# Optimization experiments

Hardware: AMD Instinct MI355X
Metric: run time of the kernel (lower is better)

The kernel has to match this reference:

```python
import jax, jax.numpy as jnp
import numpy as np

B, L, H, T, S, D = 64, 512, 768, 256, 128, 8
N = B * S            # 8192 graph nodes total
E = 16 * N           # random edges (avg degree 16)
NPD = N // D         # nodes per document
NEG_SLOPE = 0.2


def setup_inputs() -> dict:
    rng = np.random.default_rng(0)
    key = jax.random.key(0)
    ks = jax.random.split(key, 11)
    features = jax.random.normal(ks[0], (B, L, H), jnp.float32)
    starts = rng.integers(0, L - 8, (B, T))
    lens = rng.integers(1, 9, (B, T))
    token_spans = jnp.asarray(np.stack([starts, starts + lens], -1), jnp.int32)
    masks = jnp.ones((B, L), jnp.int32)
    selected_indices = jnp.asarray(rng.integers(0, T, (B, S)), jnp.int32)
    # edges within each document's node block, plus self loops (dgl.add_self_loop)
    dst0 = rng.integers(0, N, E)
    src0 = (dst0 // NPD) * NPD + rng.integers(0, NPD, E)
    loop = np.arange(N)
    src = jnp.asarray(np.concatenate([src0, loop]), jnp.int32)
    dst = jnp.asarray(np.concatenate([dst0, loop]), jnp.int32)
    spd = B // D
    doc_spans = jnp.asarray(
        np.stack([np.arange(D) * spd, (np.arange(D) + 1) * spd], -1), jnp.int32)
    segment_ids = jnp.asarray(rng.integers(0, 2, (B, L)), jnp.int32)
    is_head = jnp.asarray(rng.integers(0, 3, (B, L)), jnp.int32)
    p = lambda k, shp: jax.random.normal(k, shp, jnp.float32) * 0.05
    out = dict(features=features, token_spans=token_spans, masks=masks,
               selected_indices=selected_indices, src=src, dst=dst,
               doc_spans=doc_spans, segment_ids=segment_ids, is_head=is_head)
    for i in range(3):
        out[f"W{i}"] = p(ks[1 + 3 * i], (H, H))
        out[f"al{i}"] = p(ks[2 + 3 * i], (H,))
        out[f"ar{i}"] = p(ks[3 + 3 * i], (H,))
    return out


def _gat_layer(h, W, al, ar, src, dst, n):
    # DGL GATConv, 1 head: z = Wh; e_ij = LeakyReLU(a_l.z_i + a_r.z_j);
    # edge-softmax over incoming edges of each dst; aggregate; ELU.
    z = h @ W                                   # [N, H]
    el = z @ al                                 # [N]
    er = z @ ar                                 # [N]
    e = jax.nn.leaky_relu(el[src] + er[dst], NEG_SLOPE)
    e = e - jax.ops.segment_max(e, dst, num_segments=n)[dst]
    ex = jnp.exp(e)
    a = ex / jax.ops.segment_sum(ex, dst, num_segments=n)[dst]
    out = jax.ops.segment_sum(a[:, None] * z[src], dst, num_segments=n)
    return jax.nn.elu(out)


def reference(features, W0, al0, ar0, W1, al1, ar1, W2, al2, ar2,
              token_spans, masks, selected_indices, src, dst,
              doc_spans, segment_ids, is_head):
    dt = features.dtype
    # --- AverageSpanExtractor over token spans ---
    pos = jnp.arange(L)
    s = token_spans[..., 0:1]                   # [B,T,1]
    e = token_spans[..., 1:2]
    span_mask = ((pos >= s) & (pos < e) & (masks[:, None, :] > 0)).astype(dt)
    counts = jnp.maximum(span_mask.sum(-1), 1.0)
    token_repr = jnp.einsum('btl,blh->bth', span_mask, features) / counts[..., None]
    token_repr = token_repr * (token_spans[..., 1] > 0).astype(dt)[..., None]
    # --- select graph nodes ---
    sel = jnp.take_along_axis(token_repr, selected_indices[:, :, None], axis=1)
    h = sel.reshape(N, H)
    # --- 3-layer single-head GAT ---
    for (W, al, ar) in ((W0, al0, ar0), (W1, al1, ar1), (W2, al2, ar2)):
        h = _gat_layer(h, W, al, ar, src, dst, N)
    # --- dgl.mean_nodes per document ---
    sent_doc = jnp.searchsorted(doc_spans[:, 0], jnp.arange(B), side='right') - 1
    node_doc = sent_doc[jnp.arange(N) // S]
    node_cnt = jnp.maximum(
        jax.ops.segment_sum(jnp.ones(N, dt), node_doc, num_segments=D), 1.0)
    avg = jax.ops.segment_sum(h, node_doc, num_segments=D) / node_cnt[:, None]
    # --- query features ---
    qmask = ((is_head != 2) & (segment_ids == 0) & (masks > 0)).astype(dt)
    all_q = (features * qmask[..., None]).sum(1)   # [B,H]
    doc_cnt = jnp.maximum((doc_spans[:, 1] - doc_spans[:, 0]).astype(dt), 1.0)
    qf = jax.ops.segment_sum(all_q, sent_doc, num_segments=D) / doc_cnt[:, None]
    # --- L1 pairwise distance per document ---
    return jnp.abs(qf - avg).sum(-1)               # [D]
```

## Files before the change

### kernel.cpp

```cpp
#include <hip/hip_runtime.h>
#include <hip/hip_bf16.h>

constexpr int B_ = 64, L_ = 512, H_ = 768, T_ = 256, S_ = 128, D_ = 8;
constexpr int N_ = B_ * S_;
constexpr int E0_ = 16 * N_;
constexpr int NE_ = E0_ + N_;
constexpr float NEG_SLOPE = 0.2f;
constexpr int KDIM = 768;

typedef __attribute__((ext_vector_type(8))) short short8v;
typedef __attribute__((ext_vector_type(4))) float f32x4;

#define GLOAD_LDS16(g, l) __builtin_amdgcn_global_load_lds( \
    (const __attribute__((address_space(1))) void*)(g), \
    (__attribute__((address_space(3))) void*)(l), 16, 0, 0)

__device__ __forceinline__ float bf2f(short s) {
  unsigned u = ((unsigned)(unsigned short)s) << 16;
  return __builtin_bit_cast(float, u);
}
__device__ __forceinline__ short f2bf(float f) {
  return (short)__bfloat16_as_ushort(__float2bfloat16(f));
}
__device__ __forceinline__ int docof(int b, const int* __restrict__ doc_spans) {
  int cnt = 0;
  for (int dd = 0; dd < D_; dd++) cnt += (doc_spans[dd * 2] <= b) ? 1 : 0;
  return cnt - 1;
}

__global__ __launch_bounds__(256) void k_token_wt(const float* __restrict__ features,
                                                  const int* __restrict__ token_spans,
                                                  const int* __restrict__ masks,
                                                  const int* __restrict__ selidx,
                                                  __hip_bfloat16* __restrict__ h0,
                                                  const float* __restrict__ W0,
                                                  const float* __restrict__ W1,
                                                  const float* __restrict__ W2,
                                                  __hip_bfloat16* __restrict__ Wt) {
  int bid = blockIdx.x;
  if (bid < N_) {
    if (threadIdx.x >= 192) return;
    int n = bid;
    int b = n / S_;
    int t = selidx[n];
    int st = token_spans[(b * T_ + t) * 2 + 0];
    int en = token_spans[(b * T_ + t) * 2 + 1];
    int tid = threadIdx.x;
    float4 a = make_float4(0.f, 0.f, 0.f, 0.f);
    int cnt = 0;
    for (int l = st; l < en; l++) {
      if (masks[b * L_ + l] > 0) {
        cnt++;
        float4 v = ((const float4*)(features + ((size_t)b * L_ + l) * H_))[tid];
        a.x += v.x; a.y += v.y; a.z += v.z; a.w += v.w;
      }
    }
    float sc = (en > 0) ? (1.0f / (float)max(cnt, 1)) : 0.0f;
    short4 o;
    o.x = f2bf(a.x * sc); o.y = f2bf(a.y * sc); o.z = f2bf(a.z * sc); o.w = f2bf(a.w * sc);
    ((short4*)(h0 + (size_t)n * H_))[tid] = o;
    return;
  }
  int wb = bid - N_;
  int layer = wb / 576;
  int rem = wb % 576;
  int k0 = (rem % 24) * 32, n0 = (rem / 24) * 32;
  const float* Ws[3] = {W0, W1, W2};
  const float* W = Ws[layer];
  __hip_bfloat16* O = Wt + (size_t)layer * H_ * H_;
  __shared__ float tbuf[32][33];
  int x = threadIdx.x % 32, y = threadIdx.x / 32;
  for (int i = 0; i < 32; i += 8)
    tbuf[y + i][x] = W[(size_t)(k0 + y + i) * H_ + n0 + x];
  __syncthreads();
  for (int i = 0; i < 32; i += 8)
    O[(size_t)(n0 + y + i) * H_ + k0 + x] = __float2bfloat16(tbuf[x][y + i]);
}

__global__ void k_count(const int* __restrict__ dst, int* __restrict__ counts, int ne) {
  int i = blockIdx.x * 256 + threadIdx.x;
  if (i < ne) atomicAdd(&counts[dst[i]], 1);
}

__global__ __launch_bounds__(1024) void k_scan(const int* __restrict__ counts,
                                               int* __restrict__ offs,
                                               int* __restrict__ cursor) {
  __shared__ int part[1024];
  int tid = threadIdx.x;
  int base = tid * 8;
  int loc[8];
  int s = 0;
  for (int i = 0; i < 8; i++) { loc[i] = s; s += counts[base + i]; }
  part[tid] = s;
  __syncthreads();
  for (int off = 1; off < 1024; off <<= 1) {
    int v = (tid >= off) ? part[tid - off] : 0;
    __syncthreads();
    part[tid] += v;
    __syncthreads();
  }
  int excl = (tid == 0) ? 0 : part[tid - 1];
  for (int i = 0; i < 8; i++) {
    int o = excl + loc[i];
    offs[base + i] = o;
    cursor[base + i] = o;
  }
  if (tid == 1023) offs[N_] = part[1023];
}

__global__ void k_scatter(const int* __restrict__ dst, const int* __restrict__ src,
                          int* __restrict__ cursor, int* __restrict__ esrc, int ne) {
  int i = blockIdx.x * 256 + threadIdx.x;
  if (i < ne) { int p = atomicAdd(&cursor[dst[i]], 1); esrc[p] = src[i]; }
}

__global__ __launch_bounds__(256) void k_gemm_bf16(const __hip_bfloat16* __restrict__ A,
                                                   const __hip_bfloat16* __restrict__ Bt,
                                                   __hip_bfloat16* __restrict__ C,
                                                   const float* __restrict__ al,
                                                   const float* __restrict__ ar,
                                                   float* __restrict__ el,
                                                   float* __restrict__ er) {
  __shared__ __hip_bfloat16 As[2][128 * 32];
  __shared__ __hip_bfloat16 Bs[2][128 * 32];
  int tid = threadIdx.x;
  int bm = blockIdx.x * 128;
  int bn = blockIdx.y * 128;
  int w = tid >> 6;
  int l = tid & 63;
  int wr = w >> 1, wc = w & 1;
  int lr = l & 15;
  int lk = (l >> 4) * 8;
  f32x4 acc[4][4] = {};

  const __hip_bfloat16* gA[2];
  const __hip_bfloat16* gB[2];
  int ldsoff[2];
#pragma unroll
  for (int i = 0; i < 2; i++) {
    int idx = i * 256 + tid;
    int row = idx >> 2;
    int ck = (idx & 3) * 8;
    gA[i] = A + (size_t)(bm + row) * KDIM + ck;
    gB[i] = Bt + (size_t)(bn + row) * KDIM + ck;
    ldsoff[i] = idx * 8;
  }

  auto stage = [&](int buf, int k0) {
#pragma unroll
    for (int i = 0; i < 2; i++) GLOAD_LDS16(gA[i] + k0, &As[buf][ldsoff[i]]);
#pragma unroll
    for (int i = 0; i < 2; i++) GLOAD_LDS16(gB[i] + k0, &Bs[buf][ldsoff[i]]);
  };

  stage(0, 0);
  __syncthreads();

  constexpr int NT = KDIM / 32;
  for (int t = 0; t < NT; t++) {
    int cur = t & 1;
    if (t < NT - 1) stage(cur ^ 1, (t + 1) * 32);
    short8v a_frag[4], b_frag[4];
#pragma unroll
    for (int m = 0; m < 4; m++)
      a_frag[m] = *(const short8v*)&As[cur][(wr * 64 + m * 16 + lr) * 32 + lk];
#pragma unroll
    for (int n = 0; n < 4; n++)
      b_frag[n] = *(const short8v*)&Bs[cur][(wc * 64 + n * 16 + lr) * 32 + lk];
#pragma unroll
    for (int m = 0; m < 4; m++)
#pragma unroll
      for (int n = 0; n < 4; n++)
        acc[m][n] = __builtin_amdgcn_mfma_f32_16x16x32_bf16(a_frag[m], b_frag[n], acc[m][n], 0, 0, 0);
    __syncthreads();
  }

  float alv[4], arv[4];
#pragma unroll
  for (int n = 0; n < 4; n++) {
    int col = bn + wc * 64 + n * 16 + lr;
    alv[n] = al[col]; arv[n] = ar[col];
  }
#pragma unroll
  for (int m = 0; m < 4; m++) {
    int rbase = bm + wr * 64 + m * 16 + (l >> 4) * 4;
#pragma unroll
    for (int n = 0; n < 4; n++) {
      int col = bn + wc * 64 + n * 16 + lr;
#pragma unroll
      for (int r = 0; r < 4; r++)
        C[(size_t)(rbase + r) * H_ + col] = __float2bfloat16(acc[m][n][r]);
    }
#pragma unroll
    for (int r = 0; r < 4; r++) {
      float pel = 0.f, per_ = 0.f;
#pragma unroll
      for (int n = 0; n < 4; n++) {
        pel  += acc[m][n][r] * alv[n];
        per_ += acc[m][n][r] * arv[n];
      }
#pragma unroll
      for (int off2 = 1; off2 < 16; off2 <<= 1) {
        pel  += __shfl_xor(pel,  off2);
        per_ += __shfl_xor(per_, off2);
      }
      if (lr == 0) {
        atomicAdd(&el[rbase + r], pel);
        atomicAdd(&er[rbase + r], per_);
      }
    }
  }
}

__global__ __launch_bounds__(256) void k_agg(const __hip_bfloat16* __restrict__ z,
                                             const float* __restrict__ el,
                                             const float* __restrict__ er,
                                             const int* __restrict__ offs,
                                             const int* __restrict__ esrc,
                                             __hip_bfloat16* __restrict__ hout) {
  int wv = threadIdx.x >> 6, lane = threadIdx.x & 63;
  int n = blockIdx.x * 4 + wv;
  int o0 = offs[n];
  int deg = offs[n + 1] - o0;
  float ern = er[n];
  float acc[12] = {};

  if (deg <= 64) {
    float w_ = 0.f; int s_ = 0;
    if (lane < deg) {
      s_ = esrc[o0 + lane];
      float v = el[s_] + ern;
      w_ = v > 0.f ? v : NEG_SLOPE * v;
    } else {
      w_ = -1e30f;
    }
    float m = w_;
    for (int off = 32; off; off >>= 1) m = fmaxf(m, __shfl_xor(m, off));
    float ex = (lane < deg) ? __expf(w_ - m) : 0.f;
    float sum = ex;
    for (int off = 32; off; off >>= 1) sum += __shfl_xor(sum, off);
    w_ = ex / sum;
    for (int j = 0; j < deg; j++) {
      float wj = __shfl(w_, j);
      int sj = __shfl(s_, j);
      const short4* zr = (const short4*)(z + (size_t)sj * H_);
#pragma unroll
      for (int i = 0; i < 3; i++) {
        short4 v = zr[lane + i * 64];
        acc[i * 4 + 0] += wj * bf2f(v.x);
        acc[i * 4 + 1] += wj * bf2f(v.y);
        acc[i * 4 + 2] += wj * bf2f(v.z);
        acc[i * 4 + 3] += wj * bf2f(v.w);
      }
    }
  } else {
    float lmax = -1e30f;
    for (int i = lane; i < deg; i += 64) {
      float v = el[esrc[o0 + i]] + ern;
      v = v > 0.f ? v : NEG_SLOPE * v;
      lmax = fmaxf(lmax, v);
    }
    for (int off = 32; off; off >>= 1) lmax = fmaxf(lmax, __shfl_xor(lmax, off));
    float lsum = 0.f;
    for (int i = lane; i < deg; i += 64) {
      float v = el[esrc[o0 + i]] + ern;
      v = v > 0.f ? v : NEG_SLOPE * v;
      lsum += __expf(v - lmax);
    }
    for (int off = 32; off; off >>= 1) lsum += __shfl_xor(lsum, off);
    float inv = 1.0f / lsum;
    for (int base = 0; base < deg; base += 64) {
      int chunk = min(64, deg - base);
      float w_ = 0.f; int s_ = 0;
      if (lane < chunk) {
        s_ = esrc[o0 + base + lane];
        float v = el[s_] + ern;
        v = v > 0.f ? v : NEG_SLOPE * v;
        w_ = __expf(v - lmax) * inv;
      }
      for (int j = 0; j < chunk; j++) {
        float wj = __shfl(w_, j);
        int sj = __shfl(s_, j);
        const short4* zr = (const short4*)(z + (size_t)sj * H_);
#pragma unroll
        for (int i = 0; i < 3; i++) {
          short4 v = zr[lane + i * 64];
          acc[i * 4 + 0] += wj * bf2f(v.x);
          acc[i * 4 + 1] += wj * bf2f(v.y);
          acc[i * 4 + 2] += wj * bf2f(v.z);
          acc[i * 4 + 3] += wj * bf2f(v.w);
        }
      }
    }
  }

  short4* ho = (short4*)(hout + (size_t)n * H_);
#pragma unroll
  for (int i = 0; i < 3; i++) {
    float e0 = acc[i * 4 + 0]; e0 = e0 > 0.f ? e0 : __expf(e0) - 1.f;
    float e1 = acc[i * 4 + 1]; e1 = e1 > 0.f ? e1 : __expf(e1) - 1.f;
    float e2 = acc[i * 4 + 2]; e2 = e2 > 0.f ? e2 : __expf(e2) - 1.f;
    float e3 = acc[i * 4 + 3]; e3 = e3 > 0.f ? e3 : __expf(e3) - 1.f;
    short4 o; o.x = f2bf(e0); o.y = f2bf(e1); o.z = f2bf(e2); o.w = f2bf(e3);
    ho[lane + i * 64] = o;
  }
}

__global__ __launch_bounds__(192) void k_avgqf(const __hip_bfloat16* __restrict__ h,
                                               const float* __restrict__ features,
                                               const int* __restrict__ masks,
                                               const int* __restrict__ segment_ids,
                                               const int* __restrict__ is_head,
                                               const int* __restrict__ doc_spans,
                                               float* __restrict__ avgp,
                                               float* __restrict__ qfp) {
  int b = blockIdx.x;
  int y = blockIdx.y;
  int tid = threadIdx.x;
  int d = docof(b, doc_spans);
  if (y < 8) {
    int s0 = y * 16;
    float4 a = make_float4(0.f, 0.f, 0.f, 0.f);
    for (int i = 0; i < 16; i++) {
      short4 v = ((const short4*)(h + ((size_t)(b * S_ + s0 + i)) * H_))[tid];
      a.x += bf2f(v.x); a.y += bf2f(v.y); a.z += bf2f(v.z); a.w += bf2f(v.w);
    }
    atomicAdd(&avgp[d * H_ + tid * 4 + 0], a.x);
    atomicAdd(&avgp[d * H_ + tid * 4 + 1], a.y);
    atomicAdd(&avgp[d * H_ + tid * 4 + 2], a.z);
    atomicAdd(&avgp[d * H_ + tid * 4 + 3], a.w);
  } else {
    int l0 = (y - 8) * 16;
    __shared__ float qm[16];
    if (tid < 16) {
      int l = l0 + tid;
      qm[tid] = (is_head[b * L_ + l] != 2 && segment_ids[b * L_ + l] == 0 && masks[b * L_ + l] > 0) ? 1.0f : 0.0f;
    }
    __syncthreads();
    float4 a = make_float4(0.f, 0.f, 0.f, 0.f);
    for (int i = 0; i < 16; i++) {
      if (qm[i] != 0.f) {
        float4 v = ((const float4*)(features + ((size_t)b * L_ + l0 + i) * H_))[tid];
        a.x += v.x; a.y += v.y; a.z += v.z; a.w += v.w;
      }
    }
    atomicAdd(&qfp[d * H_ + tid * 4 + 0], a.x);
    atomicAdd(&qfp[d * H_ + tid * 4 + 1], a.y);
    atomicAdd(&qfp[d * H_ + tid * 4 + 2], a.z);
    atomicAdd(&qfp[d * H_ + tid * 4 + 3], a.w);
  }
}

__global__ __launch_bounds__(512) void k_final(const float* __restrict__ qfp,
                                               const float* __restrict__ avgp,
                                               const int* __restrict__ doc_spans,
                                               float* __restrict__ out) {
  __shared__ int ds[D_ * 2];
  int tid = threadIdx.x;
  if (tid < D_ * 2) ds[tid] = doc_spans[tid];
  __syncthreads();
  int d = tid >> 6, lane = tid & 63;
  int nsent = 0;
  for (int b = 0; b < B_; b++) {
    int cnt = 0;
#pragma unroll
    for (int dd = 0; dd < D_; dd++) cnt += (ds[dd * 2] <= b) ? 1 : 0;
    nsent += ((cnt - 1) == d) ? 1 : 0;
  }
  float inv_node = 1.0f / fmaxf((float)nsent * (float)S_, 1.0f);
  float inv_doc  = 1.0f / fmaxf((float)(ds[d * 2 + 1] - ds[d * 2]), 1.0f);
  float acc = 0.f;
  for (int h = lane; h < H_; h += 64)
    acc += fabsf(qfp[d * H_ + h] * inv_doc - avgp[d * H_ + h] * inv_node);
  for (int off = 32; off; off >>= 1) acc += __shfl_xor(acc, off);
  if (lane == 0) out[d] = acc;
}

extern "C" void kernel_launch(void* const* d_in, const int* in_sizes, int n_in,
                              void* d_out, int out_size, void* d_ws, size_t ws_size,
                              hipStream_t stream) {
  const float* features     = (const float*)d_in[0];
  const int*   token_spans  = (const int*)d_in[1];
  const int*   masks        = (const int*)d_in[2];
  const int*   selidx       = (const int*)d_in[3];
  const int*   src          = (const int*)d_in[4];
  const int*   dst          = (const int*)d_in[5];
  const int*   doc_spans    = (const int*)d_in[6];
  const int*   segment_ids  = (const int*)d_in[7];
  const int*   is_head      = (const int*)d_in[8];
  const float* Wl[3]  = {(const float*)d_in[9],  (const float*)d_in[12], (const float*)d_in[15]};
  const float* alv[3] = {(const float*)d_in[10], (const float*)d_in[13], (const float*)d_in[16]};
  const float* arv[3] = {(const float*)d_in[11], (const float*)d_in[14], (const float*)d_in[17]};
  float* out = (float*)d_out;

  char* ws = (char*)d_ws;
  size_t off = 0;
  auto alloc = [&](size_t bytes) -> void* {
    void* p = ws + off;
    off = (off + bytes + 255) & ~(size_t)255;
    return p;
  };
  __hip_bfloat16* hA = (__hip_bfloat16*)alloc((size_t)N_ * H_ * 2);
  __hip_bfloat16* hB = (__hip_bfloat16*)alloc((size_t)N_ * H_ * 2);
  __hip_bfloat16* Wt = (__hip_bfloat16*)alloc((size_t)3 * H_ * H_ * 2);
  float* avgp   = (float*)alloc((size_t)2 * D_ * H_ * 4);
  float* qfp    = avgp + (size_t)D_ * H_;
  float* el     = (float*)alloc((size_t)3 * N_ * 4);
  float* er     = (float*)alloc((size_t)3 * N_ * 4);
  int*   counts = (int*)alloc((size_t)N_ * 4);
  size_t zero_bytes = (size_t)(2 * D_ * H_ + 6 * N_ + N_) * 4;
  int*   offs   = (int*)alloc((size_t)(N_ + 1) * 4);
  int*   cursor = (int*)alloc((size_t)N_ * 4);
  int*   esrc   = (int*)alloc((size_t)NE_ * 4);

  hipMemsetAsync(avgp, 0, zero_bytes, stream);

  k_count<<<(NE_ + 255) / 256, 256, 0, stream>>>(dst, counts, NE_);
  k_scan<<<1, 1024, 0, stream>>>(counts, offs, cursor);
  k_scatter<<<(NE_ + 255) / 256, 256, 0, stream>>>(dst, src, cursor, esrc, NE_);

  k_token_wt<<<N_ + 3 * 576, 256, 0, stream>>>(features, token_spans, masks, selidx,
                                               hA, Wl[0], Wl[1], Wl[2], Wt);

  for (int i = 0; i < 3; i++) {
    k_gemm_bf16<<<dim3(N_ / 128, H_ / 128), 256, 0, stream>>>(
        hA, Wt + (size_t)i * H_ * H_, hB, alv[i], arv[i],
        el + (size_t)i * N_, er + (size_t)i * N_);
    k_agg<<<N_ / 4, 256, 0, stream>>>(hB, el + (size_t)i * N_, er + (size_t)i * N_,
                                      offs, esrc, hA);
  }

  k_avgqf<<<dim3(B_, 40), 192, 0, stream>>>(hA, features, masks, segment_ids, is_head,
                                            doc_spans, avgp, qfp);
  k_final<<<1, 512, 0, stream>>>(qfp, avgp, doc_spans, out);
}
```

Baseline: 261.5 us.

## Store GAT projections as fp8, fuse workspace zeroing, coarsen query-sum blocks

The GEMM output z is now stored as one fp8 byte per element instead of bf16, halving the bytes the gather-heavy aggregation kernel reads per neighbour. The hipMemsetAsync is replaced by extra zeroing blocks appended to the token/weight-transpose kernel, which now launches before the CSR build. The query-feature reduction uses 64-token chunks per block instead of 16, cutting atomics and block count. FP8 storage loses precision in the aggregated features and may break accuracy tolerance.

```diff
diff --git a/kernel.cpp b/kernel.cpp
--- a/kernel.cpp
+++ b/kernel.cpp
@@ -7,6 +7,8 @@
 constexpr int NE_ = E0_ + N_;
 constexpr float NEG_SLOPE = 0.2f;
 constexpr int KDIM = 768;
+constexpr int NB_WT = 3 * 576;
+constexpr int NB_ZERO = 68;
 
 typedef __attribute__((ext_vector_type(8))) short short8v;
 typedef __attribute__((ext_vector_type(4))) float f32x4;
@@ -36,7 +38,8 @@
                                                   const float* __restrict__ W0,
                                                   const float* __restrict__ W1,
                                                   const float* __restrict__ W2,
-                                                  __hip_bfloat16* __restrict__ Wt) {
+                                                  __hip_bfloat16* __restrict__ Wt,
+                                                  int4* __restrict__ zero_base) {
   int bid = blockIdx.x;
   if (bid < N_) {
     if (threadIdx.x >= 192) return;
@@ -61,20 +64,25 @@
     ((short4*)(h0 + (size_t)n * H_))[tid] = o;
     return;
   }
-  int wb = bid - N_;
-  int layer = wb / 576;
-  int rem = wb % 576;
-  int k0 = (rem % 24) * 32, n0 = (rem / 24) * 32;
-  const float* Ws[3] = {W0, W1, W2};
-  const float* W = Ws[layer];
-  __hip_bfloat16* O = Wt + (size_t)layer * H_ * H_;
-  __shared__ float tbuf[32][33];
-  int x = threadIdx.x % 32, y = threadIdx.x / 32;
-  for (int i = 0; i < 32; i += 8)
-    tbuf[y + i][x] = W[(size_t)(k0 + y + i) * H_ + n0 + x];
-  __syncthreads();
-  for (int i = 0; i < 32; i += 8)
-    O[(size_t)(n0 + y + i) * H_ + k0 + x] = __float2bfloat16(tbuf[x][y + i]);
+  if (bid < N_ + NB_WT) {
+    int wb = bid - N_;
+    int layer = wb / 576;
+    int rem = wb % 576;
+    int k0 = (rem % 24) * 32, n0 = (rem / 24) * 32;
+    const float* Ws[3] = {W0, W1, W2};
+    const float* W = Ws[layer];
+    __hip_bfloat16* O = Wt + (size_t)layer * H_ * H_;
+    __shared__ float tbuf[32][33];
+    int x = threadIdx.x % 32, y = threadIdx.x / 32;
+    for (int i = 0; i < 32; i += 8)
+      tbuf[y + i][x] = W[(size_t)(k0 + y + i) * H_ + n0 + x];
+    __syncthreads();
+    for (int i = 0; i < 32; i += 8)
+      O[(size_t)(n0 + y + i) * H_ + k0 + x] = __float2bfloat16(tbuf[x][y + i]);
+    return;
+  }
+  int zi = bid - N_ - NB_WT;
+  zero_base[zi * 256 + threadIdx.x] = make_int4(0, 0, 0, 0);
 }
 
 __global__ void k_count(const int* __restrict__ dst, int* __restrict__ counts, int ne) {
@@ -116,7 +124,7 @@
 
 __global__ __launch_bounds__(256) void k_gemm_bf16(const __hip_bfloat16* __restrict__ A,
                                                    const __hip_bfloat16* __restrict__ Bt,
-                                                   __hip_bfloat16* __restrict__ C,
+                                                   unsigned char* __restrict__ C,
                                                    const float* __restrict__ al,
                                                    const float* __restrict__ ar,
                                                    float* __restrict__ el,
@@ -188,8 +196,11 @@
     for (int n = 0; n < 4; n++) {
       int col = bn + wc * 64 + n * 16 + lr;
 #pragma unroll
-      for (int r = 0; r < 4; r++)
-        C[(size_t)(rbase + r) * H_ + col] = __float2bfloat16(acc[m][n][r]);
+      for (int r = 0; r < 4; r++) {
+        float v = acc[m][n][r];
+        int pk = __builtin_amdgcn_cvt_pk_fp8_f32(v, v, 0, false);
+        C[(size_t)(rbase + r) * H_ + col] = (unsigned char)(pk & 0xff);
+      }
     }
 #pragma unroll
     for (int r = 0; r < 4; r++) {
@@ -212,7 +223,7 @@
   }
 }
 
-__global__ __launch_bounds__(256) void k_agg(const __hip_bfloat16* __restrict__ z,
+__global__ __launch_bounds__(256) void k_agg(const unsigned char* __restrict__ z,
                                              const float* __restrict__ el,
                                              const float* __restrict__ er,
                                              const int* __restrict__ offs,
@@ -243,14 +254,14 @@
     for (int j = 0; j < deg; j++) {
       float wj = __shfl(w_, j);
       int sj = __shfl(s_, j);
-      const short4* zr = (const short4*)(z + (size_t)sj * H_);
+      const unsigned* zr = (const unsigned*)(z + (size_t)sj * H_);
 #pragma unroll
       for (int i = 0; i < 3; i++) {
-        short4 v = zr[lane + i * 64];
-        acc[i * 4 + 0] += wj * bf2f(v.x);
-        acc[i * 4 + 1] += wj * bf2f(v.y);
-        acc[i * 4 + 2] += wj * bf2f(v.z);
-        acc[i * 4 + 3] += wj * bf2f(v.w);
+        unsigned u = zr[lane + i * 64];
+        acc[i * 4 + 0] += wj * __builtin_amdgcn_cvt_f32_fp8(u, 0);
+        acc[i * 4 + 1] += wj * __builtin_amdgcn_cvt_f32_fp8(u, 1);
+        acc[i * 4 + 2] += wj * __builtin_amdgcn_cvt_f32_fp8(u, 2);
+        acc[i * 4 + 3] += wj * __builtin_amdgcn_cvt_f32_fp8(u, 3);
       }
     }
   } else {
@@ -281,14 +292,14 @@
       for (int j = 0; j < chunk; j++) {
         float wj = __shfl(w_, j);
         int sj = __shfl(s_, j);
-        const short4* zr = (const short4*)(z + (size_t)sj * H_);
+        const unsigned* zr = (const unsigned*)(z + (size_t)sj * H_);
 #pragma unroll
         for (int i = 0; i < 3; i++) {
-          short4 v = zr[lane + i * 64];
-          acc[i * 4 + 0] += wj * bf2f(v.x);
-          acc[i * 4 + 1] += wj * bf2f(v.y);
-          acc[i * 4 + 2] += wj * bf2f(v.z);
-          acc[i * 4 + 3] += wj * bf2f(v.w);
+          unsigned u = zr[lane + i * 64];
+          acc[i * 4 + 0] += wj * __builtin_amdgcn_cvt_f32_fp8(u, 0);
+          acc[i * 4 + 1] += wj * __builtin_amdgcn_cvt_f32_fp8(u, 1);
+          acc[i * 4 + 2] += wj * __builtin_amdgcn_cvt_f32_fp8(u, 2);
+          acc[i * 4 + 3] += wj * __builtin_amdgcn_cvt_f32_fp8(u, 3);
         }
       }
     }
@@ -330,15 +341,15 @@
     atomicAdd(&avgp[d * H_ + tid * 4 + 2], a.z);
     atomicAdd(&avgp[d * H_ + tid * 4 + 3], a.w);
   } else {
-    int l0 = (y - 8) * 16;
-    __shared__ float qm[16];
-    if (tid < 16) {
+    int l0 = (y - 8) * 64;
+    __shared__ float qm[64];
+    if (tid < 64) {
       int l = l0 + tid;
       qm[tid] = (is_head[b * L_ + l] != 2 && segment_ids[b * L_ + l] == 0 && masks[b * L_ + l] > 0) ? 1.0f : 0.0f;
     }
     __syncthreads();
     float4 a = make_float4(0.f, 0.f, 0.f, 0.f);
-    for (int i = 0; i < 16; i++) {
+    for (int i = 0; i < 64; i++) {
       if (qm[i] != 0.f) {
         float4 v = ((const float4*)(features + ((size_t)b * L_ + l0 + i) * H_))[tid];
         a.x += v.x; a.y += v.y; a.z += v.z; a.w += v.w;
@@ -401,26 +412,24 @@
     return p;
   };
   __hip_bfloat16* hA = (__hip_bfloat16*)alloc((size_t)N_ * H_ * 2);
-  __hip_bfloat16* hB = (__hip_bfloat16*)alloc((size_t)N_ * H_ * 2);
+  unsigned char*  hB = (unsigned char*)alloc((size_t)N_ * H_);
   __hip_bfloat16* Wt = (__hip_bfloat16*)alloc((size_t)3 * H_ * H_ * 2);
   float* avgp   = (float*)alloc((size_t)2 * D_ * H_ * 4);
   float* qfp    = avgp + (size_t)D_ * H_;
   float* el     = (float*)alloc((size_t)3 * N_ * 4);
   float* er     = (float*)alloc((size_t)3 * N_ * 4);
   int*   counts = (int*)alloc((size_t)N_ * 4);
-  size_t zero_bytes = (size_t)(2 * D_ * H_ + 6 * N_ + N_) * 4;
   int*   offs   = (int*)alloc((size_t)(N_ + 1) * 4);
   int*   cursor = (int*)alloc((size_t)N_ * 4);
   int*   esrc   = (int*)alloc((size_t)NE_ * 4);
 
-  hipMemsetAsync(avgp, 0, zero_bytes, stream);
+  k_token_wt<<<N_ + NB_WT + NB_ZERO, 256, 0, stream>>>(features, token_spans, masks, selidx,
+                                                       hA, Wl[0], Wl[1], Wl[2], Wt,
+                                                       (int4*)avgp);
 
   k_count<<<(NE_ + 255) / 256, 256, 0, stream>>>(dst, counts, NE_);
   k_scan<<<1, 1024, 0, stream>>>(counts, offs, cursor);
   k_scatter<<<(NE_ + 255) / 256, 256, 0, stream>>>(dst, src, cursor, esrc, NE_);
-
-  k_token_wt<<<N_ + 3 * 576, 256, 0, stream>>>(features, token_spans, masks, selidx,
-                                               hA, Wl[0], Wl[1], Wl[2], Wt);
 
   for (int i = 0; i < 3; i++) {
     k_gemm_bf16<<<dim3(N_ / 128, H_ / 128), 256, 0, stream>>>(
@@ -430,7 +439,7 @@
                                       offs, esrc, hA);
   }
 
-  k_avgqf<<<dim3(B_, 40), 192, 0, stream>>>(hA, features, masks, segment_ids, is_head,
+  k_avgqf<<<dim3(B_, 16), 192, 0, stream>>>(hA, features, masks, segment_ids, is_head,
                                             doc_spans, avgp, qfp);
   k_final<<<1, 512, 0, stream>>>(qfp, avgp, doc_spans, out);
 }
```

Measured after the change: 210.3 us, median of 3. -19.6%, faster.
